# Performance work log

Measured on AMD Instinct MI355X. Metric: run time of the kernel, lower is better.

Reference implementation:

```python
import jax, jax.numpy as jnp
import numpy as np

BN_EPS = 1e-5
NUM_SUBSET = 3


def setup_inputs() -> dict:
    key = jax.random.key(0)
    ks = jax.random.split(key, 6)
    N, C, T, V = 64, 192, 128, 25
    return {
        "x": jax.random.normal(ks[0], (N, C, T, V), dtype=jnp.float32),
        "Wqkv": jax.random.normal(ks[1], (3 * C, C), dtype=jnp.float32) * 0.05,
        "bqkv": jax.random.normal(ks[2], (3 * C,), dtype=jnp.float32) * 0.05,
        "Wff": jax.random.normal(ks[3], (C, C), dtype=jnp.float32) * 0.05,
        "bff": jax.random.normal(ks[4], (C,), dtype=jnp.float32) * 0.05,
        "gamma": jnp.ones((C,), dtype=jnp.float32),
        "beta": jnp.zeros((C,), dtype=jnp.float32),
        "running_mean": jnp.zeros((C,), dtype=jnp.float32),
        "running_var": jax.random.uniform(ks[5], (C,), dtype=jnp.float32) + 0.5,
    }


def reference(x, Wqkv, bqkv, Wff, bff, gamma, beta, running_mean, running_var):
    N, C, T, V = x.shape
    S = NUM_SUBSET
    mid = C // S  # mid_dim
    # 1x1 conv C -> 3C, then view (N, 3S, mid, T, V) and chunk into q,k,v
    qkv = jnp.einsum('nctv,oc->notv', x, Wqkv) + bqkv[None, :, None, None]
    qkv = qkv.reshape(N, 3 * S, mid, T, V)
    q, k, v = jnp.split(qkv, 3, axis=1)  # each (N, S, mid, T, V)
    # joint attention over V: contract channel and time, tanh instead of softmax
    att = jnp.tanh(jnp.einsum('nsctu,nsctv->nsuv', q, k) / (mid * T))  # (N,S,V,V)
    # weighted aggregation back to (N, C, T, V)
    y = jnp.einsum('nsuv,nsctv->nsctu', att, v).reshape(N, C, T, V)
    # ff_nets: 1x1 conv + BatchNorm2d (eval mode, running stats)
    y = jnp.einsum('nctv,oc->notv', y, Wff) + bff[None, :, None, None]
    inv = gamma / jnp.sqrt(running_var + BN_EPS)
    y = y * inv[None, :, None, None] + (beta - running_mean * inv)[None, :, None, None]
    # residual + LeakyReLU(0.1)
    out = jax.nn.leaky_relu(x + y, negative_slope=0.1)
    return (out, att)
```

## Files before the change

### kernel.cpp

```cpp
#include <hip/hip_runtime.h>
#include <hip/hip_bf16.h>

typedef __attribute__((ext_vector_type(8))) short bf16x8;
typedef __attribute__((ext_vector_type(4))) float f32x4;

#define MFMA16(a, b, c) __builtin_amdgcn_mfma_f32_16x16x32_bf16((a), (b), (c), 0, 0, 0)

#define N_ 64
#define C_ 192
#define T_ 128
#define V_ 25
#define S_ 3
#define MID 64
#define TV 3200
#define C3 576
#define OUT_ELEMS 39321600ULL
#define NCHUNK 16
#define PSTRIDE 640

static __device__ __forceinline__ float bf2f(ushort u) {
    union { unsigned int i; float f; } x; x.i = ((unsigned int)u) << 16; return x.f;
}
static __device__ __forceinline__ ushort f2bf(float f) {
    union { float f; unsigned int i; } x; x.f = f;
    unsigned int r = x.i + 0x7fffu + ((x.i >> 16) & 1u);
    return (ushort)(r >> 16);
}
static __device__ __forceinline__ unsigned int pack2(float a, float b) {
    return (unsigned int)f2bf(a) | ((unsigned int)f2bf(b) << 16);
}

__global__ __launch_bounds__(256) void kconv(const float* __restrict__ src,
                                             ushort* __restrict__ dst, int n4) {
    int i = blockIdx.x * 256 + threadIdx.x;
    if (i < n4) {
        float4 d = *(const float4*)(src + (size_t)i * 4);
        unsigned int* o = (unsigned int*)dst + (size_t)i * 2;
        o[0] = pack2(d.x, d.y);
        o[1] = pack2(d.z, d.w);
    }
}

__global__ __launch_bounds__(256) void k1_qkv(const float* __restrict__ x,
                                              const ushort* __restrict__ Wbf,
                                              const float* __restrict__ bias,
                                              ushort* __restrict__ qkvT) {
    int m0 = blockIdx.x * 64, n = blockIdx.y;
    __shared__ ushort As[64 * 200];
    __shared__ ushort Bs[64 * 200];
    __shared__ float biasS[64];
    unsigned int* scratchU = (unsigned int*)Bs;
    ushort* scratchS = Bs;
    int tid = threadIdx.x;

    for (int cg = 0; cg < 2; cg++) {
        if (cg) __syncthreads();
#pragma unroll
        for (int j = 0; j < 6; j++) {
            int chunk = tid + j * 256;
            int cc = chunk >> 4, m4 = chunk & 15;
            float4 d = *(const float4*)(x + ((size_t)n * C_ + cg * 96 + cc) * TV + m0 + m4 * 4);
            scratchU[cc * 35 + m4 * 2]     = pack2(d.x, d.y);
            scratchU[cc * 35 + m4 * 2 + 1] = pack2(d.z, d.w);
        }
        __syncthreads();
#pragma unroll
        for (int j = 0; j < 24; j++) {
            int idx = tid + j * 256;
            int mm = idx / 96, cc = idx % 96;
            As[mm * 200 + cg * 96 + cc] = scratchS[cc * 70 + mm];
        }
    }

    int wave = tid >> 6, lane = tid & 63;
    int mb = (wave >> 1) * 32, ob = (wave & 1) * 32;
    int lrow = lane & 15, lk = lane >> 4;

    for (int oi = 0; oi < 9; oi++) {
        int o0 = oi * 64;
        __syncthreads();
#pragma unroll
        for (int j = 0; j < 6; j++) {
            int chunk = tid + j * 256;
            int r = chunk / 24, c8 = chunk % 24;
            *(uint4*)&Bs[r * 200 + c8 * 8] =
                *(const uint4*)(Wbf + (size_t)(o0 + r) * C_ + c8 * 8);
        }
        if (tid < 64) biasS[tid] = bias[o0 + tid];
        __syncthreads();

        f32x4 acc[2][2];
#pragma unroll
        for (int i = 0; i < 2; i++)
#pragma unroll
            for (int j = 0; j < 2; j++) acc[i][j] = (f32x4){0.f, 0.f, 0.f, 0.f};

#pragma unroll
        for (int ks = 0; ks < 6; ks++) {
            bf16x8 a[2], b[2];
#pragma unroll
            for (int mt = 0; mt < 2; mt++)
                a[mt] = *(const bf16x8*)&As[(mb + mt * 16 + lrow) * 200 + ks * 32 + lk * 8];
#pragma unroll
            for (int ot = 0; ot < 2; ot++)
                b[ot] = *(const bf16x8*)&Bs[(ob + ot * 16 + lrow) * 200 + ks * 32 + lk * 8];
#pragma unroll
            for (int mt = 0; mt < 2; mt++)
#pragma unroll
                for (int ot = 0; ot < 2; ot++)
                    acc[mt][ot] = MFMA16(a[mt], b[ot], acc[mt][ot]);
        }

        ushort* op = qkvT + ((size_t)n * TV + m0) * C3 + o0;
#pragma unroll
        for (int mt = 0; mt < 2; mt++) {
#pragma unroll
            for (int ot = 0; ot < 2; ot++) {
                int o = ob + ot * 16 + lrow;
                float bv = biasS[o];
#pragma unroll
                for (int r = 0; r < 4; r++) {
                    int m = mb + mt * 16 + lk * 4 + r;
                    op[(size_t)m * C3 + o] = f2bf(acc[mt][ot][r] + bv);
                }
            }
        }
    }
}

__global__ __launch_bounds__(256) void k2_att(const ushort* __restrict__ qkvT,
                                              float* __restrict__ partial) {
    int tc = blockIdx.x, s = blockIdx.y, n = blockIdx.z;
    __shared__ ushort tiles[4 * 2 * 32 * 72];
    __shared__ float red[4 * 32 * 33];
    int tid = threadIdx.x, wave = tid >> 6, lane = tid & 63;
    ushort* myQ = &tiles[wave * 2 * 2304];
    ushort* myK = myQ + 2304;

    if (lane < 63) {
        *(uint4*)&myQ[1800 + lane * 8] = (uint4){0, 0, 0, 0};
        *(uint4*)&myK[1800 + lane * 8] = (uint4){0, 0, 0, 0};
    }

    const size_t nbase = (size_t)n * TV * C3;
    int qoff = s * MID;
    int koff = C_ + s * MID;
    int lrow = lane & 15, lk = lane >> 4;

    f32x4 acc[2][2];
#pragma unroll
    for (int i = 0; i < 2; i++)
#pragma unroll
        for (int j = 0; j < 2; j++) acc[i][j] = (f32x4){0.f, 0.f, 0.f, 0.f};

#pragma unroll
    for (int i = 0; i < 2; i++) {
        int t = tc * 8 + wave + 4 * i;
#pragma unroll
        for (int j = 0; j < 7; j++) {
            int idx = lane + j * 64;
            if (idx < 400) {
                int op = idx / 200, rr = idx % 200;
                int row = rr >> 3, c16 = rr & 7;
                int chan = (op ? koff : qoff) + c16 * 8;
                uint4 d = *(const uint4*)(qkvT + nbase + (size_t)(t * V_ + row) * C3 + chan);
                *(uint4*)((op ? myK : myQ) + row * 72 + c16 * 8) = d;
            }
        }
#pragma unroll
        for (int ks = 0; ks < 2; ks++) {
            bf16x8 a0 = *(const bf16x8*)&myQ[lrow * 72 + ks * 32 + lk * 8];
            bf16x8 a1 = *(const bf16x8*)&myQ[(16 + lrow) * 72 + ks * 32 + lk * 8];
            bf16x8 b0 = *(const bf16x8*)&myK[lrow * 72 + ks * 32 + lk * 8];
            bf16x8 b1 = *(const bf16x8*)&myK[(16 + lrow) * 72 + ks * 32 + lk * 8];
            acc[0][0] = MFMA16(a0, b0, acc[0][0]);
            acc[0][1] = MFMA16(a0, b1, acc[0][1]);
            acc[1][0] = MFMA16(a1, b0, acc[1][0]);
            acc[1][1] = MFMA16(a1, b1, acc[1][1]);
        }
    }

#pragma unroll
    for (int ub = 0; ub < 2; ub++)
#pragma unroll
        for (int vb = 0; vb < 2; vb++)
#pragma unroll
            for (int r = 0; r < 4; r++) {
                int u = ub * 16 + lk * 4 + r, v = vb * 16 + lrow;
                red[wave * 1056 + u * 33 + v] = acc[ub][vb][r];
            }
    __syncthreads();

    float* pb = partial + (((size_t)n * S_ + s) * NCHUNK + tc) * PSTRIDE;
    for (int idx = tid; idx < 1024; idx += 256) {
        int u = idx >> 5, v = idx & 31;
        if (u < V_ && v < V_) {
            float sum = red[u * 33 + v] + red[1056 + u * 33 + v] +
                        red[2112 + u * 33 + v] + red[3168 + u * 33 + v];
            pb[u * V_ + v] = sum;
        }
    }
}

__global__ __launch_bounds__(256) void k2_reduce(const float* __restrict__ partial,
                                                 float* __restrict__ attOut) {
    int idx = blockIdx.x * 256 + threadIdx.x;
    if (idx >= 192 * 625) return;
    int ns = idx / 625, r = idx % 625;
    const float* p = partial + (size_t)ns * NCHUNK * PSTRIDE + r;
    float s = 0.f;
#pragma unroll
    for (int j = 0; j < NCHUNK; j++) s += p[j * PSTRIDE];
    attOut[(size_t)ns * 625 + r] = tanhf(s * (1.0f / 8192.0f));
}

__global__ __launch_bounds__(192) void k3_y(const ushort* __restrict__ qkvT,
                                            const float* __restrict__ attF,
                                            ushort* __restrict__ yT) {
    int t = blockIdx.x, n = blockIdx.y;
    __shared__ float attS[3 * 700];
    int tid = threadIdx.x;
    const float* ab = attF + (size_t)n * (S_ * V_ * V_);
    for (int idx = tid; idx < S_ * V_ * V_; idx += 192) {
        int s = idx / 625, r = idx % 625;
        attS[s * 700 + (r / 25) * 28 + (r % 25)] = ab[idx];
    }
    __syncthreads();

    int c = tid;
    int s = c >> 6;
    const ushort* vb = qkvT + ((size_t)n * TV + (size_t)t * V_) * C3 + 2 * C_ + c;
    float vreg[25];
#pragma unroll
    for (int v = 0; v < 25; v++) vreg[v] = bf2f(vb[(size_t)v * C3]);

    ushort* yb = yT + ((size_t)n * TV + (size_t)t * V_) * C_ + c;
    const float* as = &attS[s * 700];
    for (int u = 0; u < 25; u++) {
        float a = 0.f;
#pragma unroll
        for (int v = 0; v < 25; v++) a += as[u * 28 + v] * vreg[v];
        yb[(size_t)u * C_] = f2bf(a);
    }
}

__global__ __launch_bounds__(256) void k4_out(const ushort* __restrict__ yT,
                                              const ushort* __restrict__ Wbf,
                                              const float* __restrict__ bff,
                                              const float* __restrict__ gamma,
                                              const float* __restrict__ beta,
                                              const float* __restrict__ rmean,
                                              const float* __restrict__ rvar,
                                              const float* __restrict__ x,
                                              float* __restrict__ out) {
    int m0 = blockIdx.x * 64, n = blockIdx.y;
    __shared__ ushort As[64 * 200];
    __shared__ ushort Bs[64 * 200];
    __shared__ float invS[64], shiftS[64];
    float* zT = (float*)Bs;
    int tid = threadIdx.x;

    const ushort* ab = yT + ((size_t)n * TV + m0) * C_;
#pragma unroll
    for (int j = 0; j < 6; j++) {
        int chunk = tid + j * 256;
        int r = chunk / 24, c8 = chunk % 24;
        *(uint4*)&As[r * 200 + c8 * 8] = *(const uint4*)(ab + (size_t)r * C_ + c8 * 8);
    }

    int wave = tid >> 6, lane = tid & 63;
    int mb = (wave >> 1) * 32, obw = (wave & 1) * 32;
    int lrow = lane & 15, lk = lane >> 4;

    for (int oi = 0; oi < 3; oi++) {
        int o0 = oi * 64;
        __syncthreads();
#pragma unroll
        for (int j = 0; j < 6; j++) {
            int chunk = tid + j * 256;
            int r = chunk / 24, c8 = chunk % 24;
            *(uint4*)&Bs[r * 200 + c8 * 8] =
                *(const uint4*)(Wbf + (size_t)(o0 + r) * C_ + c8 * 8);
        }
        if (tid < 64) {
            int o = o0 + tid;
            float inv = gamma[o] * rsqrtf(rvar[o] + 1e-5f);
            invS[tid] = inv;
            shiftS[tid] = beta[o] - rmean[o] * inv + bff[o] * inv;
        }
        __syncthreads();

        f32x4 acc[2][2];
#pragma unroll
        for (int i = 0; i < 2; i++)
#pragma unroll
            for (int j = 0; j < 2; j++) acc[i][j] = (f32x4){0.f, 0.f, 0.f, 0.f};

#pragma unroll
        for (int ks = 0; ks < 6; ks++) {
            bf16x8 a[2], b[2];
#pragma unroll
            for (int mt = 0; mt < 2; mt++)
                a[mt] = *(const bf16x8*)&As[(mb + mt * 16 + lrow) * 200 + ks * 32 + lk * 8];
#pragma unroll
            for (int ot = 0; ot < 2; ot++)
                b[ot] = *(const bf16x8*)&Bs[(obw + ot * 16 + lrow) * 200 + ks * 32 + lk * 8];
#pragma unroll
            for (int mt = 0; mt < 2; mt++)
#pragma unroll
                for (int ot = 0; ot < 2; ot++)
                    acc[mt][ot] = MFMA16(a[mt], b[ot], acc[mt][ot]);
        }

        __syncthreads();
#pragma unroll
        for (int mt = 0; mt < 2; mt++)
#pragma unroll
            for (int ot = 0; ot < 2; ot++) {
                int o = obw + ot * 16 + lrow;
                float inv = invS[o], sh = shiftS[o];
#pragma unroll
                for (int r = 0; r < 4; r++) {
                    int m = mb + mt * 16 + lk * 4 + r;
                    zT[o * 68 + m] = acc[mt][ot][r] * inv + sh;
                }
            }
        __syncthreads();

        const float* xb = x + ((size_t)n * C_ + o0) * TV + m0;
        float* ob2 = out + ((size_t)n * C_ + o0) * TV + m0;
#pragma unroll
        for (int j = 0; j < 4; j++) {
            int chunk = tid + j * 256;
            int o = chunk >> 4, m4 = chunk & 15;
            float4 zv = *(float4*)&zT[o * 68 + m4 * 4];
            float4 xv = *(const float4*)(xb + (size_t)o * TV + m4 * 4);
            float4 res; float a;
            a = xv.x + zv.x; res.x = (a >= 0.f) ? a : 0.1f * a;
            a = xv.y + zv.y; res.y = (a >= 0.f) ? a : 0.1f * a;
            a = xv.z + zv.z; res.z = (a >= 0.f) ? a : 0.1f * a;
            a = xv.w + zv.w; res.w = (a >= 0.f) ? a : 0.1f * a;
            *(float4*)(ob2 + (size_t)o * TV + m4 * 4) = res;
        }
    }
}

extern "C" void kernel_launch(void* const* d_in, const int* in_sizes, int n_in,
                              void* d_out, int out_size, void* d_ws, size_t ws_size,
                              hipStream_t stream) {
    (void)in_sizes; (void)n_in; (void)out_size; (void)ws_size;
    const float* x    = (const float*)d_in[0];
    const float* Wqkv = (const float*)d_in[1];
    const float* bqkv = (const float*)d_in[2];
    const float* Wff  = (const float*)d_in[3];
    const float* bff  = (const float*)d_in[4];
    const float* gam  = (const float*)d_in[5];
    const float* bet  = (const float*)d_in[6];
    const float* rme  = (const float*)d_in[7];
    const float* rva  = (const float*)d_in[8];
    float* out = (float*)d_out;
    float* attOut = out + OUT_ELEMS;

    char* ws = (char*)d_ws;
    ushort* qkvT = (ushort*)ws;
    float*  partial = (float*)(ws + 235929600);
    ushort* yT      = (ushort*)(ws + 235929600);
    ushort* WqkvB   = (ushort*)(ws + 235929600);
    ushort* WffB    = (ushort*)ws;

    kconv<<<dim3(108), 256, 0, stream>>>(Wqkv, WqkvB, 27648);
    k1_qkv<<<dim3(50, 64), 256, 0, stream>>>(x, WqkvB, bqkv, qkvT);
    k2_att<<<dim3(NCHUNK, 3, 64), 256, 0, stream>>>(qkvT, partial);
    k2_reduce<<<dim3(469), 256, 0, stream>>>(partial, attOut);
    k3_y<<<dim3(128, 64), 192, 0, stream>>>(qkvT, attOut, yT);
    kconv<<<dim3(36), 256, 0, stream>>>(Wff, WffB, 9216);
    k4_out<<<dim3(50, 64), 256, 0, stream>>>(yT, WffB, bff, gam, bet, rme, rva, x, out);
}
```

Before: 500.7 us.

## Prefetch weights into registers, load attention operands directly from global memory

In the QKV and FF GEMM kernels, the next 64-row weight tile is prefetched into registers while the current tile is computed, and bias and BN constants are staged once for all output tiles. In the FF kernel the residual x loads are issued before the epilogue's shared-memory work. The attention kernel now reads Q/K MFMA fragments straight from global memory, clamping and masking rows past V instead of going through LDS tiles. The y kernel reads attention weights from global/cache instead of staging them in shared memory. These changes aim to hide global load latency and cut LDS traffic and barriers, at the cost of more register pressure and uncoalesced direct loads.

```diff
diff --git a/kernel.cpp b/kernel.cpp
--- a/kernel.cpp
+++ b/kernel.cpp
@@ -48,10 +48,20 @@
     int m0 = blockIdx.x * 64, n = blockIdx.y;
     __shared__ ushort As[64 * 200];
     __shared__ ushort Bs[64 * 200];
-    __shared__ float biasS[64];
+    __shared__ float biasS[C3];
     unsigned int* scratchU = (unsigned int*)Bs;
     ushort* scratchS = Bs;
     int tid = threadIdx.x;
+
+    int wr[6], wc[6];
+    uint4 w[6];
+#pragma unroll
+    for (int j = 0; j < 6; j++) {
+        int chunk = tid + j * 256;
+        wr[j] = chunk / 24; wc[j] = (chunk % 24) * 8;
+        w[j] = *(const uint4*)(Wbf + (size_t)wr[j] * C_ + wc[j]);
+    }
+    for (int i = tid; i < C3; i += 256) biasS[i] = bias[i];
 
     for (int cg = 0; cg < 2; cg++) {
         if (cg) __syncthreads();
@@ -80,13 +90,13 @@
         int o0 = oi * 64;
         __syncthreads();
 #pragma unroll
-        for (int j = 0; j < 6; j++) {
-            int chunk = tid + j * 256;
-            int r = chunk / 24, c8 = chunk % 24;
-            *(uint4*)&Bs[r * 200 + c8 * 8] =
-                *(const uint4*)(Wbf + (size_t)(o0 + r) * C_ + c8 * 8);
-        }
-        if (tid < 64) biasS[tid] = bias[o0 + tid];
+        for (int j = 0; j < 6; j++)
+            *(uint4*)&Bs[wr[j] * 200 + wc[j]] = w[j];
+        if (oi < 8) {
+#pragma unroll
+            for (int j = 0; j < 6; j++)
+                w[j] = *(const uint4*)(Wbf + (size_t)(o0 + 64 + wr[j]) * C_ + wc[j]);
+        }
         __syncthreads();
 
         f32x4 acc[2][2];
@@ -117,7 +127,7 @@
 #pragma unroll
             for (int ot = 0; ot < 2; ot++) {
                 int o = ob + ot * 16 + lrow;
-                float bv = biasS[o];
+                float bv = biasS[o0 + o];
 #pragma unroll
                 for (int r = 0; r < 4; r++) {
                     int m = mb + mt * 16 + lk * 4 + r;
@@ -131,21 +141,18 @@
 __global__ __launch_bounds__(256) void k2_att(const ushort* __restrict__ qkvT,
                                               float* __restrict__ partial) {
     int tc = blockIdx.x, s = blockIdx.y, n = blockIdx.z;
-    __shared__ ushort tiles[4 * 2 * 32 * 72];
     __shared__ float red[4 * 32 * 33];
     int tid = threadIdx.x, wave = tid >> 6, lane = tid & 63;
-    ushort* myQ = &tiles[wave * 2 * 2304];
-    ushort* myK = myQ + 2304;
-
-    if (lane < 63) {
-        *(uint4*)&myQ[1800 + lane * 8] = (uint4){0, 0, 0, 0};
-        *(uint4*)&myK[1800 + lane * 8] = (uint4){0, 0, 0, 0};
-    }
+    int lrow = lane & 15, lk = lane >> 4;
 
     const size_t nbase = (size_t)n * TV * C3;
     int qoff = s * MID;
     int koff = C_ + s * MID;
-    int lrow = lane & 15, lk = lane >> 4;
+
+    int r1 = 16 + lrow;
+    int r1c = (r1 < V_) ? r1 : (V_ - 1);
+    bool r1ok = r1 < V_;
+    bf16x8 zv = {0, 0, 0, 0, 0, 0, 0, 0};
 
     f32x4 acc[2][2];
 #pragma unroll
@@ -156,23 +163,17 @@
 #pragma unroll
     for (int i = 0; i < 2; i++) {
         int t = tc * 8 + wave + 4 * i;
-#pragma unroll
-        for (int j = 0; j < 7; j++) {
-            int idx = lane + j * 64;
-            if (idx < 400) {
-                int op = idx / 200, rr = idx % 200;
-                int row = rr >> 3, c16 = rr & 7;
-                int chan = (op ? koff : qoff) + c16 * 8;
-                uint4 d = *(const uint4*)(qkvT + nbase + (size_t)(t * V_ + row) * C3 + chan);
-                *(uint4*)((op ? myK : myQ) + row * 72 + c16 * 8) = d;
-            }
-        }
+        const ushort* base0 = qkvT + nbase + (size_t)(t * V_ + lrow) * C3;
+        const ushort* base1 = qkvT + nbase + (size_t)(t * V_ + r1c) * C3;
 #pragma unroll
         for (int ks = 0; ks < 2; ks++) {
-            bf16x8 a0 = *(const bf16x8*)&myQ[lrow * 72 + ks * 32 + lk * 8];
-            bf16x8 a1 = *(const bf16x8*)&myQ[(16 + lrow) * 72 + ks * 32 + lk * 8];
-            bf16x8 b0 = *(const bf16x8*)&myK[lrow * 72 + ks * 32 + lk * 8];
-            bf16x8 b1 = *(const bf16x8*)&myK[(16 + lrow) * 72 + ks * 32 + lk * 8];
+            int co = ks * 32 + lk * 8;
+            bf16x8 a0 = *(const bf16x8*)(base0 + qoff + co);
+            bf16x8 b0 = *(const bf16x8*)(base0 + koff + co);
+            bf16x8 a1 = *(const bf16x8*)(base1 + qoff + co);
+            bf16x8 b1 = *(const bf16x8*)(base1 + koff + co);
+            a1 = r1ok ? a1 : zv;
+            b1 = r1ok ? b1 : zv;
             acc[0][0] = MFMA16(a0, b0, acc[0][0]);
             acc[0][1] = MFMA16(a0, b1, acc[0][1]);
             acc[1][0] = MFMA16(a1, b0, acc[1][0]);
@@ -218,28 +219,21 @@
                                             const float* __restrict__ attF,
                                             ushort* __restrict__ yT) {
     int t = blockIdx.x, n = blockIdx.y;
-    __shared__ float attS[3 * 700];
     int tid = threadIdx.x;
-    const float* ab = attF + (size_t)n * (S_ * V_ * V_);
-    for (int idx = tid; idx < S_ * V_ * V_; idx += 192) {
-        int s = idx / 625, r = idx % 625;
-        attS[s * 700 + (r / 25) * 28 + (r % 25)] = ab[idx];
-    }
-    __syncthreads();
-
     int c = tid;
-    int s = c >> 6;
+    int s = __builtin_amdgcn_readfirstlane(tid >> 6);
+    const float* as = attF + ((size_t)n * S_ + s) * 625;
+
     const ushort* vb = qkvT + ((size_t)n * TV + (size_t)t * V_) * C3 + 2 * C_ + c;
     float vreg[25];
 #pragma unroll
     for (int v = 0; v < 25; v++) vreg[v] = bf2f(vb[(size_t)v * C3]);
 
     ushort* yb = yT + ((size_t)n * TV + (size_t)t * V_) * C_ + c;
-    const float* as = &attS[s * 700];
     for (int u = 0; u < 25; u++) {
         float a = 0.f;
 #pragma unroll
-        for (int v = 0; v < 25; v++) a += as[u * 28 + v] * vreg[v];
+        for (int v = 0; v < 25; v++) a += as[u * 25 + v] * vreg[v];
         yb[(size_t)u * C_] = f2bf(a);
     }
 }
@@ -256,9 +250,18 @@
     int m0 = blockIdx.x * 64, n = blockIdx.y;
     __shared__ ushort As[64 * 200];
     __shared__ ushort Bs[64 * 200];
-    __shared__ float invS[64], shiftS[64];
+    __shared__ float invS[C_], shiftS[C_];
     float* zT = (float*)Bs;
     int tid = threadIdx.x;
+
+    int wr[6], wc[6];
+    uint4 w[6];
+#pragma unroll
+    for (int j = 0; j < 6; j++) {
+        int chunk = tid + j * 256;
+        wr[j] = chunk / 24; wc[j] = (chunk % 24) * 8;
+        w[j] = *(const uint4*)(Wbf + (size_t)wr[j] * C_ + wc[j]);
+    }
 
     const ushort* ab = yT + ((size_t)n * TV + m0) * C_;
 #pragma unroll
@@ -267,6 +270,11 @@
         int r = chunk / 24, c8 = chunk % 24;
         *(uint4*)&As[r * 200 + c8 * 8] = *(const uint4*)(ab + (size_t)r * C_ + c8 * 8);
     }
+    if (tid < C_) {
+        float inv = gamma[tid] * rsqrtf(rvar[tid] + 1e-5f);
+        invS[tid] = inv;
+        shiftS[tid] = beta[tid] - rmean[tid] * inv + bff[tid] * inv;
+    }
 
     int wave = tid >> 6, lane = tid & 63;
     int mb = (wave >> 1) * 32, obw = (wave & 1) * 32;
@@ -276,17 +284,12 @@
         int o0 = oi * 64;
         __syncthreads();
 #pragma unroll
-        for (int j = 0; j < 6; j++) {
-            int chunk = tid + j * 256;
-            int r = chunk / 24, c8 = chunk % 24;
-            *(uint4*)&Bs[r * 200 + c8 * 8] =
-                *(const uint4*)(Wbf + (size_t)(o0 + r) * C_ + c8 * 8);
-        }
-        if (tid < 64) {
-            int o = o0 + tid;
-            float inv = gamma[o] * rsqrtf(rvar[o] + 1e-5f);
-            invS[tid] = inv;
-            shiftS[tid] = beta[o] - rmean[o] * inv + bff[o] * inv;
+        for (int j = 0; j < 6; j++)
+            *(uint4*)&Bs[wr[j] * 200 + wc[j]] = w[j];
+        if (oi < 2) {
+#pragma unroll
+            for (int j = 0; j < 6; j++)
+                w[j] = *(const uint4*)(Wbf + (size_t)(o0 + 64 + wr[j]) * C_ + wc[j]);
         }
         __syncthreads();
 
@@ -313,12 +316,23 @@
         }
 
         __syncthreads();
+
+        const float* xb = x + ((size_t)n * C_ + o0) * TV + m0;
+        float* ob2 = out + ((size_t)n * C_ + o0) * TV + m0;
+        float4 xv[4];
+#pragma unroll
+        for (int j = 0; j < 4; j++) {
+            int chunk = tid + j * 256;
+            int o = chunk >> 4, m4 = chunk & 15;
+            xv[j] = *(const float4*)(xb + (size_t)o * TV + m4 * 4);
+        }
+
 #pragma unroll
         for (int mt = 0; mt < 2; mt++)
 #pragma unroll
             for (int ot = 0; ot < 2; ot++) {
                 int o = obw + ot * 16 + lrow;
-                float inv = invS[o], sh = shiftS[o];
+                float inv = invS[o0 + o], sh = shiftS[o0 + o];
 #pragma unroll
                 for (int r = 0; r < 4; r++) {
                     int m = mb + mt * 16 + lk * 4 + r;
@@ -327,19 +341,16 @@
             }
         __syncthreads();
 
-        const float* xb = x + ((size_t)n * C_ + o0) * TV + m0;
-        float* ob2 = out + ((size_t)n * C_ + o0) * TV + m0;
 #pragma unroll
         for (int j = 0; j < 4; j++) {
             int chunk = tid + j * 256;
             int o = chunk >> 4, m4 = chunk & 15;
             float4 zv = *(float4*)&zT[o * 68 + m4 * 4];
-            float4 xv = *(const float4*)(xb + (size_t)o * TV + m4 * 4);
             float4 res; float a;
-            a = xv.x + zv.x; res.x = (a >= 0.f) ? a : 0.1f * a;
-            a = xv.y + zv.y; res.y = (a >= 0.f) ? a : 0.1f * a;
-            a = xv.z + zv.z; res.z = (a >= 0.f) ? a : 0.1f * a;
-            a = xv.w + zv.w; res.w = (a >= 0.f) ? a : 0.1f * a;
+            a = xv[j].x + zv.x; res.x = (a >= 0.f) ? a : 0.1f * a;
+            a = xv[j].y + zv.y; res.y = (a >= 0.f) ? a : 0.1f * a;
+            a = xv[j].z + zv.z; res.z = (a >= 0.f) ? a : 0.1f * a;
+            a = xv[j].w + zv.w; res.w = (a >= 0.f) ? a : 0.1f * a;
             *(float4*)(ob2 + (size_t)o * TV + m4 * 4) = res;
         }
     }
```

Measured after the change: 685.6 us. +36.9%, slower.
